# Optimization experiments

Measured on AMD Instinct MI355X. Metric: run time of the kernel, lower is better.

## Reference

```python
import jax, jax.numpy as jnp
import numpy as np

B, S, W = 16, 512, 5
H, E, V = 512, 256, 100000


def setup_inputs() -> dict:
    key = jax.random.key(0)
    ks = jax.random.split(key, 20)
    inp = {
        "hiddens": jax.random.normal(ks[0], (B, S, H), jnp.float32),
        "masks": jax.random.randint(ks[1], (B, S), 0, 2, jnp.int32),
        "begins": jax.random.randint(ks[2], (B, S, W), 0, V, jnp.int32),
        "begin_lens": jax.random.randint(ks[3], (B, S), 0, W + 1, jnp.int32),
        "middles": jax.random.randint(ks[4], (B, S, W), 0, V, jnp.int32),
        "middle_lens": jax.random.randint(ks[5], (B, S), 0, W + 1, jnp.int32),
        "ends": jax.random.randint(ks[6], (B, S, W), 0, V, jnp.int32),
        "end_lens": jax.random.randint(ks[7], (B, S), 0, W + 1, jnp.int32),
        # parameters
        "emb": jax.random.normal(ks[8], (V, E), jnp.float32) * 0.02,
        "W_hidden": jax.random.normal(ks[9], (H, 3 * H), jnp.float32) * (1.0 / np.sqrt(H)),
        "b_hidden": jnp.zeros((3 * H,), jnp.float32),
        "W_begin": jax.random.normal(ks[10], (E, 2 * H), jnp.float32) * (1.0 / np.sqrt(E)),
        "b_begin": jnp.zeros((2 * H,), jnp.float32),
        "W_middle": jax.random.normal(ks[11], (E, 2 * H), jnp.float32) * (1.0 / np.sqrt(E)),
        "b_middle": jnp.zeros((2 * H,), jnp.float32),
        "W_end": jax.random.normal(ks[12], (E, 2 * H), jnp.float32) * (1.0 / np.sqrt(E)),
        "b_end": jnp.zeros((2 * H,), jnp.float32),
        "W_gate": jax.random.normal(ks[13], (H, 9), jnp.float32) * (1.0 / np.sqrt(H)),
        "b_gate": jnp.zeros((9,), jnp.float32),
    }
    return inp


def _len_mask(lens, w):
    # True where the lattice candidate is valid (mimics _make_mask's 1s)
    return jnp.arange(w)[None, None, :] < lens[:, :, None]


def _gates(hiddens, masks, W_gate, b_gate):
    b, s, _ = hiddens.shape
    lmr = hiddens @ W_gate + b_gate                      # (B,S,9)
    left, mid, right = jnp.split(lmr, 3, axis=-1)        # each (B,S,3)
    g = jax.nn.sigmoid(left[:, :-2] + mid[:, 1:-1] + right[:, 2:])  # (B,S-2,3)
    ones = jnp.ones((b, 1), g.dtype)
    zeros = jnp.zeros((b, 1), g.dtype)
    begin_g = jnp.concatenate([ones, g[..., 0], ones], axis=1)
    mid_g = jnp.concatenate([zeros, g[..., 1], zeros], axis=1)
    end_g = jnp.concatenate([ones, g[..., 2], ones], axis=1)
    pad = masks == 0
    z = jnp.zeros((), g.dtype)
    return (jnp.where(pad, z, begin_g), jnp.where(pad, z, mid_g), jnp.where(pad, z, end_g))


def reference(hiddens, masks, begins, begin_lens, middles, middle_lens, ends, end_lens,
              emb, W_hidden, b_hidden, W_begin, b_begin, W_middle, b_middle,
              W_end, b_end, W_gate, b_gate):
    w = begins.shape[-1]
    begin_m = _len_mask(begin_lens, w)
    middle_m = _len_mask(middle_lens, w)
    end_m = _len_mask(end_lens, w)

    begin_kv = emb[begins] @ W_begin + b_begin           # (B,S,W,2H)
    middle_kv = emb[middles] @ W_middle + b_middle
    end_kv = emb[ends] @ W_end + b_end

    query, hidden_key, hidden_value = jnp.split(hiddens @ W_hidden + b_hidden, 3, axis=-1)
    bg, mg, eg = _gates(hiddens, masks, W_gate, b_gate)
    begin_kv = bg[:, :, None, None] * begin_kv
    middle_kv = mg[:, :, None, None] * middle_kv
    end_kv = eg[:, :, None, None] * end_kv

    kv = jnp.concatenate([begin_kv, middle_kv, end_kv], axis=-2)   # (B,S,3W,2H)
    h = hiddens.shape[-1]
    keys, values = jnp.split(kv, 2, axis=-1)
    keys = jnp.concatenate([hidden_key[:, :, None, :], keys], axis=-2)     # (B,S,1+3W,H)
    values = jnp.concatenate([hidden_value[:, :, None, :], values], axis=-2)

    # combined mask: True entries get -1e10 (faithful to masked_fill_(masks, -1e10))
    score_mask = jnp.concatenate(
        [(masks != 0)[:, :, None], begin_m, middle_m, end_m], axis=-1)     # (B,S,1+3W)

    scores = jnp.einsum("bsh,bskh->bsk", query, keys)
    scores = jnp.where(score_mask, jnp.asarray(-1e10, scores.dtype), scores)
    weights = jax.nn.softmax(scores, axis=-1)
    return jnp.einsum("bsk,bskh->bsh", weights, values)
```

## Files before the change

### kernel.cpp

```cpp
#include <hip/hip_runtime.h>
#include <cstdint>
#include <cstddef>


typedef unsigned short u16;
typedef _Float16 f16;
typedef __attribute__((ext_vector_type(8))) f16 f16x8;
typedef __attribute__((ext_vector_type(4))) float f32x4;

#define MROWS 8192
#define SS 512

static __device__ __forceinline__ u16 f2h(float x) {
  f16 h = (f16)x;
  return __builtin_bit_cast(u16, h);
}
static __device__ __forceinline__ float h2f(u16 h) {
  return (float)__builtin_bit_cast(f16, h);
}
static __device__ __forceinline__ float sigm(float x) { return 1.f / (1.f + __expf(-x)); }

static __device__ __forceinline__ void gl2lds(const u16* g, u16* l) {
  __builtin_amdgcn_global_load_lds(
      (const __attribute__((address_space(1))) unsigned int*)g,
      (__attribute__((address_space(3))) unsigned int*)l, 16, 0, 0);
}

__global__ __launch_bounds__(256) void prep_all(
    const float* __restrict__ X, const float* __restrict__ Wg,
    const float* __restrict__ bg, const float* __restrict__ Wh,
    const float* __restrict__ Wb, const float* __restrict__ Wm,
    const float* __restrict__ We, const float* __restrict__ bb,
    const float* __restrict__ bm, const float* __restrict__ be,
    const float* __restrict__ bh, u16* __restrict__ Xh,
    float* __restrict__ lmr, float* __restrict__ s0, u16* __restrict__ Breg,
    u16* __restrict__ Acat, u16* __restrict__ Whq, u16* __restrict__ WvT,
    float* __restrict__ bcat, float* __restrict__ u, float* __restrict__ cbuf) {
  __shared__ float shmem[4608];
#define TI(r, c) shmem[(r)*65 + (c)]
  const int b = blockIdx.x;
  const int t = threadIdx.x;
  if (b < 64) {
    int k0 = (b & 7) * 64;
    int n0 = (b >> 3) * 64;
#pragma unroll
    for (int i = 0; i < 16; i++) {
      int li = i * 256 + t; int r = li >> 6, c = li & 63;
      TI(r, c) = Wh[(size_t)(k0 + r) * 1536 + 1024 + n0 + c];
    }
    __syncthreads();
#pragma unroll
    for (int i = 0; i < 16; i++) {
      int li = i * 256 + t; int r = li >> 6, c = li & 63;
      Breg[(size_t)(512 + n0 + r) * 512 + k0 + c] = f2h(TI(c, r));
    }
  } else if (b < 128) {
#pragma unroll
    for (int i = 0; i < 4; i++) {
      int q4 = (b - 64) * 1024 + t * 4 + i;
      int k = q4 >> 7;
      int c4 = (q4 & 127) * 4;
      float4 vq = *(const float4*)(Wh + (size_t)k * 1536 + c4);
      float4 vk = *(const float4*)(Wh + (size_t)k * 1536 + 512 + c4);
      ushort4 qh, kh;
      qh.x = f2h(vq.x); qh.y = f2h(vq.y); qh.z = f2h(vq.z); qh.w = f2h(vq.w);
      kh.x = f2h(vk.x); kh.y = f2h(vk.y); kh.z = f2h(vk.z); kh.w = f2h(vk.w);
      size_t o = (size_t)k * 512 + c4;
      *(ushort4*)(Whq + o) = qh;
      *(ushort4*)(Acat + o) = kh;
    }
  } else if (b < 576) {
    int tid = (b - 128) * 256 + t;
    int n = tid >> 7;
    int kq = (tid & 127) * 4;
    float4 v;
    if (n < 768) {
      int ty = n >> 8, c = n & 255;
      const float* src = (ty == 0 ? Wb : ty == 1 ? Wm : We) + (size_t)c * 1024 + kq;
      v = *(const float4*)src;
    } else if (n < 771) {
      int ty = n - 768;
      const float* src = (ty == 0 ? bb : ty == 1 ? bm : be) + kq;
      v = *(const float4*)src;
    } else {
      v = make_float4(0.f, 0.f, 0.f, 0.f);
    }
    ushort4 h; h.x = f2h(v.x); h.y = f2h(v.y); h.z = f2h(v.z); h.w = f2h(v.w);
    ((ushort4*)(Acat + (size_t)512 * 512))[tid] = h;
  } else if (b < 672) {
    int idx = b - 576;
    int ty = idx >> 5;
    int rem = idx & 31;
    int c0 = (rem & 3) * 64;
    int n0 = (rem >> 2) * 64;
    const float* Wsrc = ty == 0 ? Wb : ty == 1 ? Wm : We;
#pragma unroll
    for (int i = 0; i < 16; i++) {
      int li = i * 256 + t; int r = li >> 6, c = li & 63;
      TI(r, c) = Wsrc[(size_t)(c0 + r) * 1024 + 512 + n0 + c];
    }
    __syncthreads();
#pragma unroll
    for (int i = 0; i < 16; i++) {
      int li = i * 256 + t; int r = li >> 6, c = li & 63;
      WvT[(size_t)(n0 + r) * 768 + ty * 256 + c0 + c] = f2h(TI(c, r));
    }
  } else if (b < 1028) {
    const int lane = t & 63;
    const int widx = (b - 672) * 4 + (t >> 6);
    const int c = lane * 8;
    if (widx < 896) {
      int n = widx;
      float acc = 0.f;
      if (n < 771) {
        const float* src;
        if (n < 768) {
          int ty = n >> 8, ce = n & 255;
          src = (ty == 0 ? Wb : ty == 1 ? Wm : We) + (size_t)ce * 1024 + c;
        } else {
          int ty = n - 768;
          src = (ty == 0 ? bb : ty == 1 ? bm : be) + c;
        }
        float4 a0 = *(const float4*)src;
        float4 a1 = *(const float4*)(src + 4);
        float4 b0 = *(const float4*)(bh + c);
        float4 b1 = *(const float4*)(bh + c + 4);
        acc = a0.x * b0.x + a0.y * b0.y + a0.z * b0.z + a0.w * b0.w +
              a1.x * b1.x + a1.y * b1.y + a1.z * b1.z + a1.w * b1.w;
      }
#pragma unroll
      for (int o = 32; o > 0; o >>= 1) acc += __shfl_xor(acc, o);
      if (lane == 0) bcat[512 + n] = acc;
    } else if (widx < 1408) {
      int k = widx - 896;
      const float* wr = Wh + (size_t)k * 1536;
      float4 a0 = *(const float4*)(wr + c);
      float4 a1 = *(const float4*)(wr + c + 4);
      float4 a2 = *(const float4*)(wr + 512 + c);
      float4 a3 = *(const float4*)(wr + 512 + c + 4);
      float4 b0 = *(const float4*)(bh + 512 + c);
      float4 b1 = *(const float4*)(bh + 512 + c + 4);
      float4 b2 = *(const float4*)(bh + c);
      float4 b3 = *(const float4*)(bh + c + 4);
      float acc = a0.x * b0.x + a0.y * b0.y + a0.z * b0.z + a0.w * b0.w +
                  a1.x * b1.x + a1.y * b1.y + a1.z * b1.z + a1.w * b1.w +
                  a2.x * b2.x + a2.y * b2.y + a2.z * b2.z + a2.w * b2.w +
                  a3.x * b3.x + a3.y * b3.y + a3.z * b3.z + a3.w * b3.w;
#pragma unroll
      for (int o = 32; o > 0; o >>= 1) acc += __shfl_xor(acc, o);
      if (lane == 0) u[k] = acc;
    } else if (widx == 1408) {
      float4 b0 = *(const float4*)(bh + c);
      float4 b1 = *(const float4*)(bh + c + 4);
      float4 b2 = *(const float4*)(bh + 512 + c);
      float4 b3 = *(const float4*)(bh + 512 + c + 4);
      float acc = b0.x * b2.x + b0.y * b2.y + b0.z * b2.z + b0.w * b2.w +
                  b1.x * b3.x + b1.y * b3.y + b1.z * b3.z + b1.w * b3.w;
#pragma unroll
      for (int o = 32; o > 0; o >>= 1) acc += __shfl_xor(acc, o);
      if (lane == 0) cbuf[0] = acc;
    } else if (widx < 1417) {
      int i = (widx - 1409) * 64 + lane;
      bcat[i] = bh[1024 + i];
    }
  } else {
    const int xb = b - 1028;
    if (xb < 32) s0[xb * 256 + t] = 0.f;
    for (int i = t; i < 4608; i += 256) shmem[i] = Wg[i];
    __syncthreads();
    const int lane = t & 63, wid = t >> 6;
#pragma unroll
    for (int it = 0; it < 4; it++) {
      int pos = xb * 16 + it * 4 + wid;
      const float* x = X + (size_t)pos * 512 + lane * 8;
      float4 x0 = *(const float4*)x;
      float4 x1 = *(const float4*)(x + 4);
      float xs[8] = {x0.x, x0.y, x0.z, x0.w, x1.x, x1.y, x1.z, x1.w};
      ushort4 h0, h1;
      h0.x = f2h(xs[0]); h0.y = f2h(xs[1]); h0.z = f2h(xs[2]); h0.w = f2h(xs[3]);
      h1.x = f2h(xs[4]); h1.y = f2h(xs[5]); h1.z = f2h(xs[6]); h1.w = f2h(xs[7]);
      ((ushort4*)Xh)[pos * 128 + lane * 2] = h0;
      ((ushort4*)Xh)[pos * 128 + lane * 2 + 1] = h1;
      float p[9];
#pragma unroll
      for (int c = 0; c < 9; c++) p[c] = 0.f;
      const float* wrow = shmem + (lane * 8) * 9;
#pragma unroll
      for (int j = 0; j < 8; j++)
#pragma unroll
        for (int c = 0; c < 9; c++) p[c] += xs[j] * wrow[j * 9 + c];
#pragma unroll
      for (int c = 0; c < 9; c++)
#pragma unroll
        for (int o = 32; o > 0; o >>= 1) p[c] += __shfl_xor(p[c], o);
      if (lane == 0) {
#pragma unroll
        for (int c = 0; c < 9; c++) lmr[(size_t)pos * 9 + c] = p[c] + bg[c];
      }
    }
  }
#undef TI
}

template <int MODE>
__global__ __launch_bounds__(256) void gemm_k(
    const u16* __restrict__ A, const u16* __restrict__ Bt,
    const float* __restrict__ ubias, const float* __restrict__ bcat,
    float* __restrict__ Cf, u16* __restrict__ Cb, int Kdim,
    const u16* __restrict__ Xh, float* __restrict__ s0,
    const float4* __restrict__ sc4, const u16* __restrict__ HPb,
    const float* __restrict__ bb, const float* __restrict__ bm,
    const float* __restrict__ be) {
  __shared__ __align__(16) u16 As[128 * 32];
  __shared__ __align__(16) u16 Bs[128 * 32];

  const int t = threadIdx.x;
  const int lane = t & 63;
  const int wid = t >> 6;
  const int m0 = blockIdx.x * 128;
  const int n0 = blockIdx.y * 128;
  const int wm = (wid & 1) * 64;
  const int wn = (wid >> 1) * 64;
  const int fr = lane & 15;
  const int kq = (lane >> 4) * 8;

  f32x4 acc[4][4];
#pragma unroll
  for (int i = 0; i < 4; i++)
#pragma unroll
    for (int j = 0; j < 4; j++) acc[i][j] = (f32x4){0.f, 0.f, 0.f, 0.f};

  for (int k0 = 0; k0 < Kdim; k0 += 32) {
    __syncthreads();
#pragma unroll
    for (int p = 0; p < 2; p++) {
      int li = p * 256 + t;
      int row = li >> 2;
      int so = (li & 3) * 8;
      gl2lds(&A[(size_t)(m0 + row) * Kdim + k0 + so], &As[li * 8]);
      gl2lds(&Bt[(size_t)(n0 + row) * Kdim + k0 + so], &Bs[li * 8]);
    }
    __syncthreads();
    f16x8 av[4], bv[4];
#pragma unroll
    for (int i = 0; i < 4; i++) {
      av[i] = *(const f16x8*)&As[(wm + i * 16 + fr) * 32 + kq];
      bv[i] = *(const f16x8*)&Bs[(wn + i * 16 + fr) * 32 + kq];
    }
#pragma unroll
    for (int mt = 0; mt < 4; mt++)
#pragma unroll
      for (int nt = 0; nt < 4; nt++)
        acc[mt][nt] = __builtin_amdgcn_mfma_f32_16x16x32_f16(
            av[mt], bv[nt], acc[mt][nt], 0, 0, 0);
  }

  const int r0 = (lane >> 4) * 4;
  if constexpr (MODE == 0) {
    if (blockIdx.y < 4) {
      float pl[4][4];
#pragma unroll
      for (int mt = 0; mt < 4; mt++)
#pragma unroll
        for (int r = 0; r < 4; r++) pl[mt][r] = 0.f;
#pragma unroll
      for (int mt = 0; mt < 4; mt++)
#pragma unroll
        for (int nt = 0; nt < 4; nt++) {
          int col = n0 + wn + nt * 16 + fr;
          float bv2 = ubias[col];
#pragma unroll
          for (int r = 0; r < 4; r++) {
            int row = m0 + wm + mt * 16 + r0 + r;
            pl[mt][r] += (acc[mt][nt][r] + bv2) * h2f(Xh[(size_t)row * 512 + col]);
          }
        }
#pragma unroll
      for (int mt = 0; mt < 4; mt++)
#pragma unroll
        for (int r = 0; r < 4; r++) {
          float p = pl[mt][r];
          p += __shfl_xor(p, 1);
          p += __shfl_xor(p, 2);
          p += __shfl_xor(p, 4);
          p += __shfl_xor(p, 8);
          if (fr == r) {
            int row = m0 + wm + mt * 16 + r0 + r;
            atomicAdd(&s0[row], p);
          }
        }
      return;
    }
#pragma unroll
    for (int mt = 0; mt < 4; mt++)
#pragma unroll
      for (int nt = 0; nt < 4; nt++) {
        int col = n0 - 512 + wn + nt * 16 + fr;
        float bv2 = bcat[col];
#pragma unroll
        for (int r = 0; r < 4; r++) {
          int row = m0 + wm + mt * 16 + r0 + r;
          Cb[(size_t)row * 1408 + col] = f2h(acc[mt][nt][r] + bv2);
        }
      }
  } else if constexpr (MODE == 1) {
#pragma unroll
    for (int mt = 0; mt < 4; mt++)
#pragma unroll
      for (int nt = 0; nt < 4; nt++) {
        int col = n0 + wn + nt * 16 + fr;
#pragma unroll
        for (int r = 0; r < 4; r++) {
          int row = m0 + wm + mt * 16 + r0 + r;
          int orow = row < 512 ? row : row + 512;
          Cb[(size_t)orow * 512 + col] = f2h(acc[mt][nt][r]);
        }
      }
  } else {
#pragma unroll
    for (int mt = 0; mt < 4; mt++)
#pragma unroll
      for (int nt = 0; nt < 4; nt++) {
        int col = n0 + wn + nt * 16 + fr;
        float b0 = bb[512 + col];
        float b1 = bm[512 + col];
        float b2 = be[512 + col];
#pragma unroll
        for (int r = 0; r < 4; r++) {
          int row = m0 + wm + mt * 16 + r0 + r;
          float4 s = sc4[row];
          float hv = h2f(HPb[(size_t)row * 1408 + col]);
          Cf[(size_t)row * 512 + col] =
              s.x * hv + s.y * b0 + s.z * b1 + s.w * b2 + acc[mt][nt][r];
        }
      }
  }
}

__global__ __launch_bounds__(256) void attn_kernel(
    const int* __restrict__ masks, const int* __restrict__ begins,
    const int* __restrict__ blens, const int* __restrict__ middles,
    const int* __restrict__ mlens, const int* __restrict__ ends,
    const int* __restrict__ elens, const float* __restrict__ emb,
    const u16* __restrict__ HPb, const float* __restrict__ lmr,
    const float* __restrict__ s0buf, const float* __restrict__ cbuf,
    float4* __restrict__ sc4, u16* __restrict__ Ebar) {
  const int t = threadIdx.x;
  const int lane = t & 63;
  const int wid = t >> 6;
  const int pos = blockIdx.x * 4 + wid;
  const int mask = masks[pos];
  u16* erow = Ebar + (size_t)pos * 768;

  int l0 = min(blens[pos], 5), l1 = min(mlens[pos], 5), l2 = min(elens[pos], 5);
  int nv = l0 + l1 + l2;

  if (mask == 0) {
    float s0 = s0buf[pos] + cbuf[0];
    int ninv = 15 - nv;
    float w0;
    if (ninv == 0) {
      w0 = 1.f;
    } else {
      float Mx = fmaxf(s0, 0.f);
      float e0 = __expf(s0 - Mx);
      w0 = e0 / (e0 + (float)ninv * __expf(-Mx));
    }
    if (lane == 0) sc4[pos] = make_float4(w0, 0.f, 0.f, 0.f);
    ushort4 zz; zz.x = zz.y = zz.z = zz.w = 0;
    *(ushort4*)(erow + 0 * 256 + lane * 4) = zz;
    *(ushort4*)(erow + 1 * 256 + lane * 4) = zz;
    *(ushort4*)(erow + 2 * 256 + lane * 4) = zz;
  } else {
    const int s = pos & (SS - 1);
    float g[3];
    if (s == 0 || s == SS - 1) {
      g[0] = 1.f; g[1] = 0.f; g[2] = 1.f;
    } else {
      const float* p0 = lmr + (size_t)(pos - 1) * 9;
      const float* p1 = lmr + (size_t)pos * 9;
      const float* p2 = lmr + (size_t)(pos + 1) * 9;
      g[0] = sigm(p0[0] + p1[3] + p2[6]);
      g[1] = sigm(p0[1] + p1[4] + p2[7]);
      g[2] = sigm(p0[2] + p1[5] + p2[8]);
    }
    const bool deg = (nv == 15);
    int l[3] = {l0, l1, l2};
    if (deg) { l[0] = 0; l[1] = 0; l[2] = 0; }

    float4 Pt[3];
    float qb[3];
    if (!deg) {
      const u16* prow = HPb + (size_t)pos * 1408 + 512;
#pragma unroll
      for (int ty = 0; ty < 3; ty++) {
        ushort4 pu = *(const ushort4*)(prow + ty * 256 + lane * 4);
        Pt[ty].x = h2f(pu.x); Pt[ty].y = h2f(pu.y);
        Pt[ty].z = h2f(pu.z); Pt[ty].w = h2f(pu.w);
        qb[ty] = h2f(prow[768 + ty]);
      }
    }
    const int* idxp[3];
    idxp[0] = begins + (size_t)pos * 5;
    idxp[1] = middles + (size_t)pos * 5;
    idxp[2] = ends + (size_t)pos * 5;

    float4 ev[3][5];
    float scv[3][5];
    float Mx = deg ? 0.f : -3.0e38f;
#pragma unroll
    for (int ty = 0; ty < 3; ty++) {
#pragma unroll
      for (int w = 0; w < 5; w++) {
        bool act = (w >= l[ty]);
        if (act) {
          ev[ty][w] = *(const float4*)(emb + (size_t)idxp[ty][w] * 256 + lane * 4);
          float sv = 0.f;
          if (!deg) {
            float4 e = ev[ty][w];
            float d = Pt[ty].x * e.x + Pt[ty].y * e.y + Pt[ty].z * e.z + Pt[ty].w * e.w;
#pragma unroll
            for (int o = 32; o > 0; o >>= 1) d += __shfl_xor(d, o);
            sv = g[ty] * (d + qb[ty]);
          }
          scv[ty][w] = sv;
          Mx = fmaxf(Mx, sv);
        }
      }
    }
    float wts0 = deg ? 1.f : 0.f;
    float zs = wts0;
    float wts[3][5];
#pragma unroll
    for (int ty = 0; ty < 3; ty++)
#pragma unroll
      for (int w = 0; w < 5; w++) {
        bool act = (w >= l[ty]);
        float wv = act ? __expf(scv[ty][w] - Mx) : 0.f;
        wts[ty][w] = wv;
        zs += wv;
      }
    float inv = 1.f / zs;
    float alpha[3];
#pragma unroll
    for (int ty = 0; ty < 3; ty++) {
      float ax = 0.f, ay = 0.f, az = 0.f, aw = 0.f, asum = 0.f;
#pragma unroll
      for (int w = 0; w < 5; w++) {
        if (w >= l[ty]) {
          float wk = wts[ty][w];
          asum += wk;
          ax += wk * ev[ty][w].x;
          ay += wk * ev[ty][w].y;
          az += wk * ev[ty][w].z;
          aw += wk * ev[ty][w].w;
        }
      }
      float sg = g[ty] * inv;
      alpha[ty] = sg * asum;
      ushort4 h;
      h.x = f2h(ax * sg); h.y = f2h(ay * sg); h.z = f2h(az * sg); h.w = f2h(aw * sg);
      *(ushort4*)(erow + ty * 256 + lane * 4) = h;
    }
    if (lane == 0) sc4[pos] = make_float4(wts0 * inv, alpha[0], alpha[1], alpha[2]);
  }
}

extern "C" void kernel_launch(void* const* d_in, const int* in_sizes, int n_in,
                              void* d_out, int out_size, void* d_ws, size_t ws_size,
                              hipStream_t stream) {
  const float* hiddens = (const float*)d_in[0];
  const int* masks = (const int*)d_in[1];
  const int* begins = (const int*)d_in[2];
  const int* blens = (const int*)d_in[3];
  const int* middles = (const int*)d_in[4];
  const int* mlens = (const int*)d_in[5];
  const int* ends = (const int*)d_in[6];
  const int* elens = (const int*)d_in[7];
  const float* emb = (const float*)d_in[8];
  const float* Wh = (const float*)d_in[9];
  const float* bh = (const float*)d_in[10];
  const float* Wb = (const float*)d_in[11];
  const float* bb = (const float*)d_in[12];
  const float* Wm = (const float*)d_in[13];
  const float* bm = (const float*)d_in[14];
  const float* We = (const float*)d_in[15];
  const float* be = (const float*)d_in[16];
  const float* Wg = (const float*)d_in[17];
  const float* bg = (const float*)d_in[18];
  float* out = (float*)d_out;

  char* ws = (char*)d_ws;
  size_t off = 0;
  auto alloc = [&](size_t bytes) -> char* {
    char* p = ws + off;
    off += (bytes + 255) & ~(size_t)255;
    return p;
  };
  u16* Xh = (u16*)alloc((size_t)8192 * 512 * 2);
  u16* Whq = (u16*)alloc((size_t)512 * 512 * 2);
  u16* Acat = (u16*)alloc((size_t)1408 * 512 * 2);
  u16* Breg = (u16*)alloc((size_t)1920 * 512 * 2);
  u16* WvT = (u16*)alloc((size_t)512 * 768 * 2);
  u16* HPb = (u16*)alloc((size_t)8192 * 1408 * 2);
  float* lmr = (float*)alloc((size_t)8192 * 9 * 4);
  float* s0 = (float*)alloc((size_t)8192 * 4);
  float* bcat = (float*)alloc((size_t)1408 * 4);
  float* u = (float*)alloc((size_t)512 * 4);
  float* cbuf = (float*)alloc((size_t)4);
  float* sc4 = (float*)alloc((size_t)8192 * 4 * 4);
  u16* Ebar = (u16*)alloc((size_t)8192 * 768 * 2);
  if (off > ws_size) return;

  prep_all<<<1540, 256, 0, stream>>>(hiddens, Wg, bg, Wh, Wb, Wm, We, bb, bm, be,
                                     bh, Xh, lmr, s0, Breg, Acat, Whq, WvT,
                                     bcat, u, cbuf);
  gemm_k<1><<<dim3(11, 4), 256, 0, stream>>>(
      Acat, Whq, nullptr, nullptr, nullptr, Breg, 512, nullptr, nullptr,
      nullptr, nullptr, nullptr, nullptr, nullptr);
  gemm_k<0><<<dim3(64, 15), 256, 0, stream>>>(
      Xh, Breg, u, bcat, nullptr, HPb, 512, Xh, s0,
      nullptr, nullptr, nullptr, nullptr, nullptr);
  attn_kernel<<<2048, 256, 0, stream>>>(masks, begins, blens, middles, mlens,
                                        ends, elens, emb, HPb, lmr, s0, cbuf,
                                        (float4*)sc4, Ebar);
  gemm_k<2><<<dim3(64, 4), 256, 0, stream>>>(
      Ebar, WvT, nullptr, nullptr, out, nullptr, 768, nullptr, nullptr,
      (const float4*)sc4, HPb, bb, bm, be);
}
```

Before: 288.0 us.

## Compact rows by mask so projection GEMM skips tiles unused by each branch

Adds a ballot/atomic compaction pass in the prep kernel that sorts positions into mask==0 rows (front) and mask!=0 rows (back), producing idx/perm maps. The big projection GEMM then gathers A rows through idx and early-exits tiles whose rows only belong to the branch that does not use that output slice (s0 columns for unmasked rows, P columns for masked rows). The attention kernel reads s0 and P through perm. It also doubles the K step per LDS stage to 64, which halves the number of barriers. The cost is gathered, less coalesced A loads, an extra memset and atomics, and a data-dependent set of active blocks.

```diff
diff --git a/kernel.cpp b/kernel.cpp
--- a/kernel.cpp
+++ b/kernel.cpp
@@ -32,10 +32,12 @@
     const float* __restrict__ Wb, const float* __restrict__ Wm,
     const float* __restrict__ We, const float* __restrict__ bb,
     const float* __restrict__ bm, const float* __restrict__ be,
-    const float* __restrict__ bh, u16* __restrict__ Xh,
-    float* __restrict__ lmr, float* __restrict__ s0, u16* __restrict__ Breg,
-    u16* __restrict__ Acat, u16* __restrict__ Whq, u16* __restrict__ WvT,
-    float* __restrict__ bcat, float* __restrict__ u, float* __restrict__ cbuf) {
+    const float* __restrict__ bh, const int* __restrict__ masks,
+    u16* __restrict__ Xh, float* __restrict__ lmr, float* __restrict__ s0,
+    u16* __restrict__ Breg, u16* __restrict__ Acat, u16* __restrict__ Whq,
+    u16* __restrict__ WvT, float* __restrict__ bcat, float* __restrict__ u,
+    float* __restrict__ cbuf, int* __restrict__ idx, int* __restrict__ perm,
+    int* __restrict__ cnts) {
   __shared__ float shmem[4608];
 #define TI(r, c) shmem[(r)*65 + (c)]
   const int b = blockIdx.x;
@@ -88,9 +90,9 @@
     ushort4 h; h.x = f2h(v.x); h.y = f2h(v.y); h.z = f2h(v.z); h.w = f2h(v.w);
     ((ushort4*)(Acat + (size_t)512 * 512))[tid] = h;
   } else if (b < 672) {
-    int idx = b - 576;
-    int ty = idx >> 5;
-    int rem = idx & 31;
+    int idx2 = b - 576;
+    int ty = idx2 >> 5;
+    int rem = idx2 & 31;
     int c0 = (rem & 3) * 64;
     int n0 = (rem >> 2) * 64;
     const float* Wsrc = ty == 0 ? Wb : ty == 1 ? Wm : We;
@@ -163,7 +165,7 @@
       int i = (widx - 1409) * 64 + lane;
       bcat[i] = bh[1024 + i];
     }
-  } else {
+  } else if (b < 1540) {
     const int xb = b - 1028;
     if (xb < 32) s0[xb * 256 + t] = 0.f;
     for (int i = t; i < 4608; i += 256) shmem[i] = Wg[i];
@@ -198,6 +200,25 @@
         for (int c = 0; c < 9; c++) lmr[(size_t)pos * 9 + c] = p[c] + bg[c];
       }
     }
+  } else {
+    const int lane = t & 63;
+    const int pos = (b - 1540) * 256 + t;
+    bool is0 = masks[pos] == 0;
+    unsigned long long bal = __ballot(is0);
+    unsigned long long below = (lane == 0) ? 0ull : (~0ull >> (64 - lane));
+    int rank0 = __popcll(bal & below);
+    int rank1 = __popcll((~bal) & below);
+    int n0w = __popcll(bal);
+    int base0 = 0, base1 = 0;
+    if (lane == 0) {
+      base0 = atomicAdd(&cnts[0], n0w);
+      base1 = atomicAdd(&cnts[1], 64 - n0w);
+    }
+    base0 = __shfl(base0, 0);
+    base1 = __shfl(base1, 0);
+    int slot = is0 ? (base0 + rank0) : (8191 - (base1 + rank1));
+    perm[pos] = slot;
+    idx[slot] = pos;
   }
 #undef TI
 }
@@ -207,18 +228,39 @@
     const u16* __restrict__ A, const u16* __restrict__ Bt,
     const float* __restrict__ ubias, const float* __restrict__ bcat,
     float* __restrict__ Cf, u16* __restrict__ Cb, int Kdim,
-    const u16* __restrict__ Xh, float* __restrict__ s0,
+    const u16* __restrict__ Xh, float* __restrict__ s0c,
+    const int* __restrict__ idx, const int* __restrict__ cnts,
     const float4* __restrict__ sc4, const u16* __restrict__ HPb,
     const float* __restrict__ bb, const float* __restrict__ bm,
     const float* __restrict__ be) {
-  __shared__ __align__(16) u16 As[128 * 32];
-  __shared__ __align__(16) u16 Bs[128 * 32];
+  __shared__ __align__(16) u16 As[2 * 128 * 32];
+  __shared__ __align__(16) u16 Bs[2 * 128 * 32];
 
   const int t = threadIdx.x;
   const int lane = t & 63;
   const int wid = t >> 6;
   const int m0 = blockIdx.x * 128;
   const int n0 = blockIdx.y * 128;
+
+  bool remap = false;
+  if constexpr (MODE == 0) {
+    const int cnt0 = cnts[0];
+    if (blockIdx.y < 4) {
+      if (m0 >= cnt0) return;
+      remap = true;
+    } else if (blockIdx.y >= 8) {
+      if (m0 + 128 <= cnt0) return;
+      remap = true;
+    }
+  }
+
+  int ra0 = m0 + (t >> 2), ra1 = m0 + 64 + (t >> 2);
+  if (MODE == 0 && remap) { ra0 = idx[ra0]; ra1 = idx[ra1]; }
+  const int rb0 = n0 + (t >> 2), rb1 = n0 + 64 + (t >> 2);
+  const int koff = (t & 3) * 8;
+  const int lds0 = (t >> 2) * 32 + koff;
+  const int lds1 = 2048 + lds0;
+
   const int wm = (wid & 1) * 64;
   const int wn = (wid >> 1) * 64;
   const int fr = lane & 15;
@@ -230,39 +272,46 @@
 #pragma unroll
     for (int j = 0; j < 4; j++) acc[i][j] = (f32x4){0.f, 0.f, 0.f, 0.f};
 
-  for (int k0 = 0; k0 < Kdim; k0 += 32) {
+  for (int k0 = 0; k0 < Kdim; k0 += 64) {
     __syncthreads();
 #pragma unroll
-    for (int p = 0; p < 2; p++) {
-      int li = p * 256 + t;
-      int row = li >> 2;
-      int so = (li & 3) * 8;
-      gl2lds(&A[(size_t)(m0 + row) * Kdim + k0 + so], &As[li * 8]);
-      gl2lds(&Bt[(size_t)(n0 + row) * Kdim + k0 + so], &Bs[li * 8]);
+    for (int pn = 0; pn < 2; pn++) {
+      const int kb = k0 + pn * 32 + koff;
+      gl2lds(&A[(size_t)ra0 * Kdim + kb], &As[pn * 4096 + lds0]);
+      gl2lds(&A[(size_t)ra1 * Kdim + kb], &As[pn * 4096 + lds1]);
+      gl2lds(&Bt[(size_t)rb0 * Kdim + kb], &Bs[pn * 4096 + lds0]);
+      gl2lds(&Bt[(size_t)rb1 * Kdim + kb], &Bs[pn * 4096 + lds1]);
     }
     __syncthreads();
-    f16x8 av[4], bv[4];
-#pragma unroll
-    for (int i = 0; i < 4; i++) {
-      av[i] = *(const f16x8*)&As[(wm + i * 16 + fr) * 32 + kq];
-      bv[i] = *(const f16x8*)&Bs[(wn + i * 16 + fr) * 32 + kq];
-    }
-#pragma unroll
-    for (int mt = 0; mt < 4; mt++)
-#pragma unroll
-      for (int nt = 0; nt < 4; nt++)
-        acc[mt][nt] = __builtin_amdgcn_mfma_f32_16x16x32_f16(
-            av[mt], bv[nt], acc[mt][nt], 0, 0, 0);
+#pragma unroll
+    for (int pn = 0; pn < 2; pn++) {
+      f16x8 av[4], bv[4];
+#pragma unroll
+      for (int i = 0; i < 4; i++) {
+        av[i] = *(const f16x8*)&As[pn * 4096 + (wm + i * 16 + fr) * 32 + kq];
+        bv[i] = *(const f16x8*)&Bs[pn * 4096 + (wn + i * 16 + fr) * 32 + kq];
+      }
+#pragma unroll
+      for (int mt = 0; mt < 4; mt++)
+#pragma unroll
+        for (int nt = 0; nt < 4; nt++)
+          acc[mt][nt] = __builtin_amdgcn_mfma_f32_16x16x32_f16(
+              av[mt], bv[nt], acc[mt][nt], 0, 0, 0);
+    }
   }
 
   const int r0 = (lane >> 4) * 4;
   if constexpr (MODE == 0) {
     if (blockIdx.y < 4) {
       float pl[4][4];
+      int xrow[4][4];
 #pragma unroll
       for (int mt = 0; mt < 4; mt++)
 #pragma unroll
-        for (int r = 0; r < 4; r++) pl[mt][r] = 0.f;
+        for (int r = 0; r < 4; r++) {
+          pl[mt][r] = 0.f;
+          xrow[mt][r] = idx[m0 + wm + mt * 16 + r0 + r];
+        }
 #pragma unroll
       for (int mt = 0; mt < 4; mt++)
 #pragma unroll
@@ -270,10 +319,9 @@
           int col = n0 + wn + nt * 16 + fr;
           float bv2 = ubias[col];
 #pragma unroll
-          for (int r = 0; r < 4; r++) {
-            int row = m0 + wm + mt * 16 + r0 + r;
-            pl[mt][r] += (acc[mt][nt][r] + bv2) * h2f(Xh[(size_t)row * 512 + col]);
-          }
+          for (int r = 0; r < 4; r++)
+            pl[mt][r] += (acc[mt][nt][r] + bv2) *
+                         h2f(Xh[(size_t)xrow[mt][r] * 512 + col]);
         }
 #pragma unroll
       for (int mt = 0; mt < 4; mt++)
@@ -285,24 +333,39 @@
           p += __shfl_xor(p, 4);
           p += __shfl_xor(p, 8);
           if (fr == r) {
+            int slot = m0 + wm + mt * 16 + r0 + r;
+            atomicAdd(&s0c[slot], p);
+          }
+        }
+      return;
+    }
+    if (blockIdx.y < 8) {
+#pragma unroll
+      for (int mt = 0; mt < 4; mt++)
+#pragma unroll
+        for (int nt = 0; nt < 4; nt++) {
+          int col = n0 - 512 + wn + nt * 16 + fr;
+          float bv2 = bcat[col];
+#pragma unroll
+          for (int r = 0; r < 4; r++) {
             int row = m0 + wm + mt * 16 + r0 + r;
-            atomicAdd(&s0[row], p);
+            Cb[(size_t)row * 1408 + col] = f2h(acc[mt][nt][r] + bv2);
           }
         }
-      return;
-    }
-#pragma unroll
-    for (int mt = 0; mt < 4; mt++)
-#pragma unroll
-      for (int nt = 0; nt < 4; nt++) {
-        int col = n0 - 512 + wn + nt * 16 + fr;
-        float bv2 = bcat[col];
-#pragma unroll
-        for (int r = 0; r < 4; r++) {
-          int row = m0 + wm + mt * 16 + r0 + r;
-          Cb[(size_t)row * 1408 + col] = f2h(acc[mt][nt][r] + bv2);
-        }
-      }
+    } else {
+#pragma unroll
+      for (int mt = 0; mt < 4; mt++)
+#pragma unroll
+        for (int nt = 0; nt < 4; nt++) {
+          int pcol = n0 - 1024 + wn + nt * 16 + fr;
+          float bv2 = bcat[512 + pcol];
+#pragma unroll
+          for (int r = 0; r < 4; r++) {
+            int slot = m0 + wm + mt * 16 + r0 + r;
+            Cb[(size_t)slot * 1408 + 512 + pcol] = f2h(acc[mt][nt][r] + bv2);
+          }
+        }
+    }
   } else if constexpr (MODE == 1) {
 #pragma unroll
     for (int mt = 0; mt < 4; mt++)
@@ -344,19 +407,21 @@
     const int* __restrict__ elens, const float* __restrict__ emb,
     const u16* __restrict__ HPb, const float* __restrict__ lmr,
     const float* __restrict__ s0buf, const float* __restrict__ cbuf,
-    float4* __restrict__ sc4, u16* __restrict__ Ebar) {
+    const int* __restrict__ perm, float4* __restrict__ sc4,
+    u16* __restrict__ Ebar) {
   const int t = threadIdx.x;
   const int lane = t & 63;
   const int wid = t >> 6;
   const int pos = blockIdx.x * 4 + wid;
   const int mask = masks[pos];
+  const int slot = perm[pos];
   u16* erow = Ebar + (size_t)pos * 768;
 
   int l0 = min(blens[pos], 5), l1 = min(mlens[pos], 5), l2 = min(elens[pos], 5);
   int nv = l0 + l1 + l2;
 
   if (mask == 0) {
-    float s0 = s0buf[pos] + cbuf[0];
+    float s0 = s0buf[slot] + cbuf[0];
     int ninv = 15 - nv;
     float w0;
     if (ninv == 0) {
@@ -391,7 +456,7 @@
     float4 Pt[3];
     float qb[3];
     if (!deg) {
-      const u16* prow = HPb + (size_t)pos * 1408 + 512;
+      const u16* prow = HPb + (size_t)slot * 1408 + 512;
 #pragma unroll
       for (int ty = 0; ty < 3; ty++) {
         ushort4 pu = *(const ushort4*)(prow + ty * 256 + lane * 4);
@@ -504,27 +569,31 @@
   u16* WvT = (u16*)alloc((size_t)512 * 768 * 2);
   u16* HPb = (u16*)alloc((size_t)8192 * 1408 * 2);
   float* lmr = (float*)alloc((size_t)8192 * 9 * 4);
-  float* s0 = (float*)alloc((size_t)8192 * 4);
+  float* s0c = (float*)alloc((size_t)8192 * 4);
   float* bcat = (float*)alloc((size_t)1408 * 4);
   float* u = (float*)alloc((size_t)512 * 4);
   float* cbuf = (float*)alloc((size_t)4);
   float* sc4 = (float*)alloc((size_t)8192 * 4 * 4);
   u16* Ebar = (u16*)alloc((size_t)8192 * 768 * 2);
+  int* idx = (int*)alloc((size_t)8192 * 4);
+  int* perm = (int*)alloc((size_t)8192 * 4);
+  int* cnts = (int*)alloc((size_t)256);
   if (off > ws_size) return;
 
-  prep_all<<<1540, 256, 0, stream>>>(hiddens, Wg, bg, Wh, Wb, Wm, We, bb, bm, be,
-                                     bh, Xh, lmr, s0, Breg, Acat, Whq, WvT,
-                                     bcat, u, cbuf);
+  hipMemsetAsync(cnts, 0, 8, stream);
+  prep_all<<<1572, 256, 0, stream>>>(hiddens, Wg, bg, Wh, Wb, Wm, We, bb, bm, be,
+                                     bh, masks, Xh, lmr, s0c, Breg, Acat, Whq,
+                                     WvT, bcat, u, cbuf, idx, perm, cnts);
   gemm_k<1><<<dim3(11, 4), 256, 0, stream>>>(
       Acat, Whq, nullptr, nullptr, nullptr, Breg, 512, nullptr, nullptr,
-      nullptr, nullptr, nullptr, nullptr, nullptr);
+      nullptr, nullptr, nullptr, nullptr, nullptr, nullptr, nullptr);
   gemm_k<0><<<dim3(64, 15), 256, 0, stream>>>(
-      Xh, Breg, u, bcat, nullptr, HPb, 512, Xh, s0,
+      Xh, Breg, u, bcat, nullptr, HPb, 512, Xh, s0c, idx, cnts,
       nullptr, nullptr, nullptr, nullptr, nullptr);
   attn_kernel<<<2048, 256, 0, stream>>>(masks, begins, blens, middles, mlens,
-                                        ends, elens, emb, HPb, lmr, s0, cbuf,
-                                        (float4*)sc4, Ebar);
+                                        ends, elens, emb, HPb, lmr, s0c, cbuf,
+                                        perm, (float4*)sc4, Ebar);
   gemm_k<2><<<dim3(64, 4), 256, 0, stream>>>(
       Ebar, WvT, nullptr, nullptr, out, nullptr, 768, nullptr, nullptr,
-      (const float4*)sc4, HPb, bb, bm, be);
-}
+      nullptr, nullptr, (const float4*)sc4, HPb, bb, bm, be);
+}
```

Result: faster. 282.3 us (-2.0%).
